# Kernel optimization log

Measured on AMD Instinct MI355X. Metric: run time of the kernel, lower is better.

The kernel has to match this reference:

```python
import jax, jax.numpy as jnp
import numpy as np

R = 4          # args.search_range
D = 2 * R + 1  # window size per axis -> D*D = 81 output channels


def setup_inputs() -> dict:
    key = jax.random.key(0)
    k1, k2 = jax.random.split(key)
    B, C, H, W = 4, 128, 64, 128
    src = jax.random.normal(k1, (B, C, H, W), dtype=jnp.float32)
    tgt = jax.random.normal(k2, (B, C, H, W), dtype=jnp.float32)
    return {"src": src, "tgt": tgt}


def reference(src, tgt):
    # Faithful to the torch code: tgt is zero-padded by R on each spatial side,
    # then for output pixel (i, j) the window indices into the PADDED tensor are
    # I in [i-R, i+R], J in [j-R, j+R]. For i < R the index is negative, which in
    # torch wraps around -> reproduce with modular indexing.
    B, C, H, W = src.shape
    tp = jnp.pad(tgt, ((0, 0), (0, 0), (R, R), (R, R)))  # [B,C,H+2R,W+2R]
    Hp, Wp = H + 2 * R, W + 2 * R
    # col_idx[dj, j] = (j - R + dj) mod Wp
    col_idx = (jnp.arange(W)[None, :] - R + jnp.arange(D)[:, None]) % Wp  # [D,W]
    outs = []
    for di in range(D):  # small fixed loop over 9 row offsets
        row_idx = (jnp.arange(H) - R + di) % Hp        # [H]
        t_rows = tp[:, :, row_idx, :]                  # [B,C,H,Wp]
        t_win = t_rows[:, :, :, col_idx]               # [B,C,H,D,W]
        # channel-dot-product per pixel and per column offset
        outs.append(jnp.einsum('bchdw,bchw->bdhw', t_win, src))
    # channel ordering k = di*D + dj matches the original double loop over (I, J)
    return jnp.concatenate(outs, axis=1)  # [B, D*D, H, W]
```

## Files before the change

kernel.cpp:

```cpp
#include <hip/hip_runtime.h>
#include <stdint.h>

#define NB 4
#define NC 128
#define NH 64
#define NW 128
#define HW (NH * NW)
#define ND 9
#define NOUT (ND * ND)
#define PLANE 16384
#define TGT_OFF ((size_t)NB * NH * PLANE)

typedef __attribute__((ext_vector_type(8))) short short8;
typedef __attribute__((ext_vector_type(4))) float f32x4;

__device__ __forceinline__ ushort f2bf(float f) {
  uint u = __float_as_uint(f);
  u += 0x7FFFu + ((u >> 16) & 1u);
  return (ushort)(u >> 16);
}

__global__ __launch_bounds__(512, 2) void convert_kernel(const float* __restrict__ src,
                                                         const float* __restrict__ tgt,
                                                         ushort* __restrict__ ws) {
  __shared__ ushort pl[PLANE];
  const int t   = blockIdx.x >> 8;
  const int b   = (blockIdx.x >> 6) & 3;
  const int row = blockIdx.x & 63;
  const float* in = (t ? tgt : src) + (size_t)(b * NC) * HW + row * NW;
  ushort* outp = ws + (t ? TGT_OFF : 0) + (size_t)(b * NH + row) * PLANE;

#pragma unroll
  for (int i = 0; i < 8; ++i) {
    const int cell = i * 512 + threadIdx.x;
    const int c0 = (cell >> 7) << 2;
    const int w  = cell & 127;
    ushort4 e;
    e.x = f2bf(in[(size_t)(c0 + 0) * HW + w]);
    e.y = f2bf(in[(size_t)(c0 + 1) * HW + w]);
    e.z = f2bf(in[(size_t)(c0 + 2) * HW + w]);
    e.w = f2bf(in[(size_t)(c0 + 3) * HW + w]);
    *(ushort4*)&pl[(c0 >> 3) * 1024 + w * 8 + (c0 & 7)] = e;
  }
  __syncthreads();
#pragma unroll
  for (int i = 0; i < 4; ++i) {
    const int idx = i * 512 + threadIdx.x;
    *(uint4*)(outp + idx * 8) = *(const uint4*)&pl[idx * 8];
  }
}

__global__ __launch_bounds__(512, 2) void costvol_kernel(const ushort* __restrict__ ws,
                                                         float* __restrict__ out) {
  __shared__ float outlds[ND * NW];
  const int tid  = threadIdx.x;
  const int lane = tid & 63;
  const int wave = tid >> 6;
  const int col  = lane & 15;
  const int g    = lane >> 4;

  const int xcd = blockIdx.x & 7;
  const int k   = blockIdx.x >> 3;
  const int b   = xcd >> 1;
  const int h   = ((xcd & 1) << 5) | (k / ND);
  const int di  = k % ND;
  const int y   = h + di - 8;

  if (y < 0) {
    if (tid < ND * 32) {
      const int dj = tid >> 5;
      const int w  = (tid & 31) << 2;
      f32x4 o = {0.f, 0.f, 0.f, 0.f};
      *(f32x4*)(out + ((size_t)((b * NOUT + di * ND + dj) * NH + h)) * NW + w) = o;
    }
    return;
  }

  const ushort* ap = ws + (size_t)(b * NH + h) * PLANE;
  const ushort* tp = ws + TGT_OFF + (size_t)(b * NH + y) * PLANE;
  const int m0 = wave << 4;

  short8 A[4], BD[4], BS[4];
#pragma unroll
  for (int kk = 0; kk < 4; ++kk) {
    const int off = (4 * kk + g) * 1024 + (m0 + col) * 8;
    A[kk]  = *(const short8*)&ap[off];
    BD[kk] = *(const short8*)&tp[off];
  }
  if (wave) {
#pragma unroll
    for (int kk = 0; kk < 4; ++kk)
      BS[kk] = *(const short8*)&tp[(4 * kk + g) * 1024 + (m0 - 16 + col) * 8];
  }

  f32x4 accD = {0.f, 0.f, 0.f, 0.f};
  f32x4 accS = {0.f, 0.f, 0.f, 0.f};
#pragma unroll
  for (int kk = 0; kk < 4; ++kk)
    accD = __builtin_amdgcn_mfma_f32_16x16x32_bf16(A[kk], BD[kk], accD, 0, 0, 0);
  if (wave) {
#pragma unroll
    for (int kk = 0; kk < 4; ++kk)
      accS = __builtin_amdgcn_mfma_f32_16x16x32_bf16(A[kk], BS[kk], accS, 0, 0, 0);
  }

#pragma unroll
  for (int q = 0; q < 4; ++q) {
    const int row = 4 * g + q;
    const int w   = m0 + row;
    const int djd = col - row + 8;
    if (djd >= 0 && djd <= 8)
      outlds[djd * NW + ((w + 4 * djd) & 127)] = accD[q];
    if (wave) {
      const int djs = col - row - 8;
      if (djs >= 0 && djs <= 8)
        outlds[djs * NW + ((w + 4 * djs) & 127)] = accS[q];
    }
  }
  __syncthreads();

  if (tid < ND * 32) {
    const int dj = tid >> 5;
    const int w  = (tid & 31) << 2;
    f32x4 o = *(const f32x4*)&outlds[dj * NW + ((w + 4 * dj) & 127)];
#pragma unroll
    for (int i = 0; i < 4; ++i)
      if (w + i + dj < 8) o[i] = 0.f;
    *(f32x4*)(out + ((size_t)((b * NOUT + di * ND + dj) * NH + h)) * NW + w) = o;
  }
}

extern "C" void kernel_launch(void* const* d_in, const int* in_sizes, int n_in,
                              void* d_out, int out_size, void* d_ws, size_t ws_size,
                              hipStream_t stream) {
  const float* src = (const float*)d_in[0];
  const float* tgt = (const float*)d_in[1];
  float* out = (float*)d_out;
  ushort* ws = (ushort*)d_ws;
  convert_kernel<<<dim3(2 * NB * NH), dim3(512), 0, stream>>>(src, tgt, ws);
  costvol_kernel<<<dim3(NB * NH * ND), dim3(512), 0, stream>>>(ws, out);
}
```

Measured before the change: 89.29 us.

## Process all nine row offsets per block, reusing the source fragment

Each cost-volume block now loops over all nine row offsets for one (batch, row) pair instead of launching one block per offset. The source A fragment is loaded once and reused across offsets, and the per-offset results are staged in a larger LDS buffer before one combined write-out. This cuts redundant source loads and block launch overhead. In exchange the grid shrinks from 2304 to 256 blocks, which may underfill the GPU, and LDS use grows about ninefold.

Result: no change. 90.84 us (+1.7%).

```diff
diff --git a/kernel.cpp b/kernel.cpp
--- a/kernel.cpp
+++ b/kernel.cpp
@@ -10,6 +10,7 @@
 #define NOUT (ND * ND)
 #define PLANE 16384
 #define TGT_OFF ((size_t)NB * NH * PLANE)
+#define TILE (ND * NW)
 
 typedef __attribute__((ext_vector_type(8))) short short8;
 typedef __attribute__((ext_vector_type(4))) float f32x4;
@@ -52,7 +53,7 @@
 
 __global__ __launch_bounds__(512, 2) void costvol_kernel(const ushort* __restrict__ ws,
                                                          float* __restrict__ out) {
-  __shared__ float outlds[ND * NW];
+  __shared__ float outlds[ND * TILE];
   const int tid  = threadIdx.x;
   const int lane = tid & 63;
   const int wave = tid >> 6;
@@ -60,72 +61,75 @@
   const int g    = lane >> 4;
 
   const int xcd = blockIdx.x & 7;
-  const int k   = blockIdx.x >> 3;
   const int b   = xcd >> 1;
-  const int h   = ((xcd & 1) << 5) | (k / ND);
-  const int di  = k % ND;
-  const int y   = h + di - 8;
+  const int h   = ((xcd & 1) << 5) | (blockIdx.x >> 3);
 
-  if (y < 0) {
-    if (tid < ND * 32) {
-      const int dj = tid >> 5;
-      const int w  = (tid & 31) << 2;
-      f32x4 o = {0.f, 0.f, 0.f, 0.f};
-      *(f32x4*)(out + ((size_t)((b * NOUT + di * ND + dj) * NH + h)) * NW + w) = o;
+  const ushort* ap = ws + (size_t)(b * NH + h) * PLANE;
+  const ushort* tb = ws + TGT_OFF + (size_t)(b * NH) * PLANE;
+  const int m0 = wave << 4;
+
+  short8 A[4];
+#pragma unroll
+  for (int kk = 0; kk < 4; ++kk)
+    A[kk] = *(const short8*)&ap[(4 * kk + g) * 1024 + (m0 + col) * 8];
+
+#pragma unroll
+  for (int di = 0; di < ND; ++di) {
+    const int y = h + di - 8;
+    if (y >= 0) {
+      const ushort* tp = tb + (size_t)y * PLANE;
+      short8 BD[4], BS[4];
+#pragma unroll
+      for (int kk = 0; kk < 4; ++kk) {
+        const int off = (4 * kk + g) * 1024 + (m0 + col) * 8;
+        BD[kk] = *(const short8*)&tp[off];
+      }
+      if (wave) {
+#pragma unroll
+        for (int kk = 0; kk < 4; ++kk)
+          BS[kk] = *(const short8*)&tp[(4 * kk + g) * 1024 + (m0 - 16 + col) * 8];
+      }
+
+      f32x4 accD = {0.f, 0.f, 0.f, 0.f};
+      f32x4 accS = {0.f, 0.f, 0.f, 0.f};
+#pragma unroll
+      for (int kk = 0; kk < 4; ++kk)
+        accD = __builtin_amdgcn_mfma_f32_16x16x32_bf16(A[kk], BD[kk], accD, 0, 0, 0);
+      if (wave) {
+#pragma unroll
+        for (int kk = 0; kk < 4; ++kk)
+          accS = __builtin_amdgcn_mfma_f32_16x16x32_bf16(A[kk], BS[kk], accS, 0, 0, 0);
+      }
+
+      float* ol = &outlds[di * TILE];
+#pragma unroll
+      for (int q = 0; q < 4; ++q) {
+        const int row = 4 * g + q;
+        const int w   = m0 + row;
+        const int djd = col - row + 8;
+        if (djd >= 0 && djd <= 8)
+          ol[djd * NW + ((w + 4 * djd) & 127)] = accD[q];
+        if (wave) {
+          const int djs = col - row - 8;
+          if (djs >= 0 && djs <= 8)
+            ol[djs * NW + ((w + 4 * djs) & 127)] = accS[q];
+        }
+      }
     }
-    return;
   }
 
-  const ushort* ap = ws + (size_t)(b * NH + h) * PLANE;
-  const ushort* tp = ws + TGT_OFF + (size_t)(b * NH + y) * PLANE;
-  const int m0 = wave << 4;
-
-  short8 A[4], BD[4], BS[4];
-#pragma unroll
-  for (int kk = 0; kk < 4; ++kk) {
-    const int off = (4 * kk + g) * 1024 + (m0 + col) * 8;
-    A[kk]  = *(const short8*)&ap[off];
-    BD[kk] = *(const short8*)&tp[off];
-  }
-  if (wave) {
-#pragma unroll
-    for (int kk = 0; kk < 4; ++kk)
-      BS[kk] = *(const short8*)&tp[(4 * kk + g) * 1024 + (m0 - 16 + col) * 8];
-  }
-
-  f32x4 accD = {0.f, 0.f, 0.f, 0.f};
-  f32x4 accS = {0.f, 0.f, 0.f, 0.f};
-#pragma unroll
-  for (int kk = 0; kk < 4; ++kk)
-    accD = __builtin_amdgcn_mfma_f32_16x16x32_bf16(A[kk], BD[kk], accD, 0, 0, 0);
-  if (wave) {
-#pragma unroll
-    for (int kk = 0; kk < 4; ++kk)
-      accS = __builtin_amdgcn_mfma_f32_16x16x32_bf16(A[kk], BS[kk], accS, 0, 0, 0);
-  }
-
-#pragma unroll
-  for (int q = 0; q < 4; ++q) {
-    const int row = 4 * g + q;
-    const int w   = m0 + row;
-    const int djd = col - row + 8;
-    if (djd >= 0 && djd <= 8)
-      outlds[djd * NW + ((w + 4 * djd) & 127)] = accD[q];
-    if (wave) {
-      const int djs = col - row - 8;
-      if (djs >= 0 && djs <= 8)
-        outlds[djs * NW + ((w + 4 * djs) & 127)] = accS[q];
-    }
-  }
   __syncthreads();
 
-  if (tid < ND * 32) {
-    const int dj = tid >> 5;
-    const int w  = (tid & 31) << 2;
-    f32x4 o = *(const f32x4*)&outlds[dj * NW + ((w + 4 * dj) & 127)];
+  for (int s = tid; s < ND * ND * 32; s += 512) {
+    const int di = s / (ND * 32);
+    const int r  = s % (ND * 32);
+    const int dj = r >> 5;
+    const int w  = (r & 31) << 2;
+    f32x4 o = *(const f32x4*)&outlds[di * TILE + dj * NW + ((w + 4 * dj) & 127)];
+    const bool vb = (h + di - 8) >= 0;
 #pragma unroll
     for (int i = 0; i < 4; ++i)
-      if (w + i + dj < 8) o[i] = 0.f;
+      if (!vb || (w + i + dj < 8)) o[i] = 0.f;
     *(f32x4*)(out + ((size_t)((b * NOUT + di * ND + dj) * NH + h)) * NW + w) = o;
   }
 }
@@ -138,5 +142,5 @@
   float* out = (float*)d_out;
   ushort* ws = (ushort*)d_ws;
   convert_kernel<<<dim3(2 * NB * NH), dim3(512), 0, stream>>>(src, tgt, ws);
-  costvol_kernel<<<dim3(NB * NH * ND), dim3(512), 0, stream>>>(ws, out);
+  costvol_kernel<<<dim3(NB * NH), dim3(512), 0, stream>>>(ws, out);
 }
```
